# Performance work log

Hardware: AMD Instinct MI355X
Metric: run time of the kernel (lower is better)

## Reference

```python
import jax, jax.numpy as jnp
import numpy as np

B, S, D = 4, 2048, 1024
H = 8
HD = D // H            # 128 head dim
FF = 4096 // H         # 512 per-head expert hidden
E = 8                  # num experts
K = 2                  # top-k
MU, GAMMA = 0.7, 1.0
LN_EPS = 1e-5


def setup_inputs() -> dict:
    key = jax.random.key(0)
    ks = jax.random.split(key, 12)
    sc = lambda *shape: 1.0 / np.sqrt(shape[0])
    return {
        "x": jax.random.normal(ks[0], (B, S, D), jnp.float32),
        "momentum": jnp.zeros((B * S * H, HD), jnp.float32),
        # split proj (input_dim -> input_dim)
        "split_W": jax.random.normal(ks[1], (D, D), jnp.float32) * sc(D),
        "split_b": jnp.zeros((D,), jnp.float32),
        # gate (head_dim -> num_experts)
        "gate_W": jax.random.normal(ks[2], (HD, E), jnp.float32) * sc(HD),
        "gate_b": jnp.zeros((E,), jnp.float32),
        # stacked experts: Linear(HD->FF) ReLU Linear(FF->HD)
        "W1": jax.random.normal(ks[3], (E, HD, FF), jnp.float32) * sc(HD),
        "b1": jnp.zeros((E, FF), jnp.float32),
        "W2": jax.random.normal(ks[4], (E, FF, HD), jnp.float32) * sc(FF),
        "b2": jnp.zeros((E, HD), jnp.float32),
        # layernorm over head_dim
        "ln_g": jnp.ones((HD,), jnp.float32),
        "ln_b": jnp.zeros((HD,), jnp.float32),
        # merge proj
        "merge_W": jax.random.normal(ks[5], (D, D), jnp.float32) * sc(D),
        "merge_b": jnp.zeros((D,), jnp.float32),
    }


def _topk_gate(t, gate_W, gate_b):
    # t: [T, HD] -> dense gate weights [T, E] with only top-K nonzero
    logits = t @ gate_W + gate_b                       # [T, E]
    topv, topi = jax.lax.top_k(logits, K)              # [T, K]
    gates_k = jax.nn.softmax(topv, axis=-1)            # softmax over kept experts
    onehot = jax.nn.one_hot(topi, E, dtype=t.dtype)    # [T, K, E]
    return jnp.einsum("tk,tke->te", gates_k, onehot)   # scatter back


def reference(x, momentum, split_W, split_b, gate_W, gate_b,
              W1, b1, W2, b2, ln_g, ln_b, merge_W, merge_b):
    # split: [B,S,D] -> [B*S*H, HD]
    x_hat = x @ split_W + split_b
    t = x_hat.reshape(B * S * H, HD)

    gates = _topk_gate(t, gate_W, gate_b)              # [T, E]

    # all-experts dense compute (matches the source's per-expert loop)
    h = jax.nn.relu(jnp.einsum("td,edf->etf", t, W1) + b1[:, None, :])  # [E,T,FF]
    eo = jnp.einsum("etf,efd->etd", h, W2) + b2[:, None, :]             # [E,T,HD]
    expert_outputs = jnp.einsum("te,etd->td", gates, eo)                # [T,HD]

    new_momentum = -expert_outputs + MU * momentum
    out = t + GAMMA * new_momentum

    # layernorm over head_dim
    mean = out.mean(-1, keepdims=True)
    var = out.var(-1, keepdims=True)
    out = (out - mean) * jax.lax.rsqrt(var + LN_EPS) * ln_g + ln_b

    # merge: [T,HD] -> [B,S,D] -> linear
    o = out.reshape(B, S, D)
    final = o @ merge_W + merge_b
    return final, new_momentum
```

## Files before the change

### kernel.cpp

```cpp
#include <hip/hip_runtime.h>

#define NBATCH 4
#define NS 2048
#define ND 1024
#define NH 8
#define HD 128
#define NFF 512
#define NE 8
#define NT 65536
#define NBS 8192
#define MU_F 0.7f
#define LN_EPS_F 1e-5f

typedef __attribute__((ext_vector_type(4))) float f32x4;
typedef __attribute__((ext_vector_type(2))) double f64x2;
typedef __attribute__((ext_vector_type(8))) _Float16 f16x8;
typedef __attribute__((ext_vector_type(4))) _Float16 f16x4;
typedef __attribute__((ext_vector_type(2))) _Float16 f16x2;

__device__ __forceinline__ void gload_lds16(const void* g, void* l) {
  __builtin_amdgcn_global_load_lds(
      (const __attribute__((address_space(1))) unsigned int*)g,
      (__attribute__((address_space(3))) unsigned int*)l, 16, 0, 0);
}

__global__ void zero_cnt_kernel(int* cnt) {
  cnt[threadIdx.x] = 0;
}

__global__ void tr_cvt_kernel(const float* __restrict__ in, _Float16* __restrict__ out, int R, int C) {
  __shared__ float tile[32][33];
  int b = blockIdx.z;
  const float* inp = in + (size_t)b * R * C;
  _Float16* outp = out + (size_t)b * R * C;
  int c = blockIdx.x * 32 + threadIdx.x;
  int r0 = blockIdx.y * 32;
  #pragma unroll
  for (int i = 0; i < 4; i++) {
    int r = r0 + threadIdx.y + i * 8;
    tile[threadIdx.y + i * 8][threadIdx.x] = inp[(size_t)r * C + c];
  }
  __syncthreads();
  int rr = r0 + threadIdx.x;
  #pragma unroll
  for (int i = 0; i < 4; i++) {
    int cc = blockIdx.x * 32 + threadIdx.y + i * 8;
    outp[(size_t)cc * R + rr] = (_Float16)tile[threadIdx.x][threadIdx.y + i * 8];
  }
}

__global__ void build_G_kernel(const float* __restrict__ split_W, const float* __restrict__ split_b,
                               const float* __restrict__ gate_W, const float* __restrict__ gate_b,
                               f64x2* __restrict__ Gx2, double* __restrict__ gbias) {
  int idx = blockIdx.x * 256 + threadIdx.x;
  int kp = idx >> 6, o = idx & 63, h = o >> 3, e = o & 7;
  int d0 = kp * 2;
  double a0 = 0.0, a1 = 0.0;
  const float* r0 = split_W + (size_t)d0 * ND + h * 128;
  const float* r1 = r0 + ND;
  for (int j = 0; j < 128; j++) {
    double w = (double)gate_W[j * 8 + e];
    a0 += (double)r0[j] * w;
    a1 += (double)r1[j] * w;
  }
  f64x2 gv = { a0, a1 };
  Gx2[idx] = gv;
  if (idx < 64) {
    double bacc = 0.0;
    for (int j = 0; j < 128; j++)
      bacc += (double)split_b[h * 128 + j] * (double)gate_W[j * 8 + e];
    gbias[idx] = bacc + (double)gate_b[e];
  }
}

__global__ __launch_bounds__(256) void gate_kernel(const float* __restrict__ x,
    const f64x2* __restrict__ Gx2, const double* __restrict__ gbias,
    _Float16* __restrict__ x_h,
    float* __restrict__ tkw, int* __restrict__ lists, int* __restrict__ cnt) {
  __shared__ double xsd[16][66];
  __shared__ double lg[16 * 64];
  __shared__ int lcnt[8];
  __shared__ int lbase[8];
  int tid = threadIdx.x, lane = tid & 63, w = tid >> 6;
  int bs0 = blockIdx.x * 16;
  double acc[4];
  #pragma unroll
  for (int r = 0; r < 4; r++) acc[r] = 0.0;
  int xrow = tid >> 4, xc4 = tid & 15;
  const double* xr = &xsd[0][0] + (w * 4) * 66;
  if (tid < 8) lcnt[tid] = 0;

  for (int ch = 0; ch < 16; ch++) {
    __syncthreads();
    float4 xv4 = *(const float4*)(x + (size_t)(bs0 + xrow) * ND + ch * 64 + xc4 * 4);
    f64x2 xa = { (double)xv4.x, (double)xv4.y };
    f64x2 xb = { (double)xv4.z, (double)xv4.w };
    *(f64x2*)&xsd[xrow][xc4 * 4]     = xa;
    *(f64x2*)&xsd[xrow][xc4 * 4 + 2] = xb;
    f16x4 xh = { (_Float16)xv4.x, (_Float16)xv4.y, (_Float16)xv4.z, (_Float16)xv4.w };
    *(f16x4*)(x_h + (size_t)(bs0 + xrow) * ND + ch * 64 + xc4 * 4) = xh;
    __syncthreads();
    const f64x2* Gc = Gx2 + (size_t)(ch * 32) * 64 + lane;
    #pragma unroll 8
    for (int kp = 0; kp < 32; kp++) {
      f64x2 g = Gc[kp * 64];
      #pragma unroll
      for (int r = 0; r < 4; r++) {
        f64x2 xv = *(const f64x2*)(xr + r * 66 + kp * 2);
        acc[r] += xv.x * g.x;
        acc[r] += xv.y * g.y;
      }
    }
  }
  double gb = gbias[lane];
  #pragma unroll
  for (int r = 0; r < 4; r++)
    lg[(w * 4 + r) * 64 + lane] = acc[r] + gb;
  __syncthreads();

  int i1 = 0, i2 = 0, token = 0, p1 = 0, p2 = 0;
  if (tid < 128) {
    int row = tid >> 3, h = tid & 7;
    const double* L = lg + row * 64 + h * 8;
    double v1 = L[0];
    #pragma unroll
    for (int e2 = 1; e2 < 8; e2++) if (L[e2] > v1) { v1 = L[e2]; i1 = e2; }
    i2 = -1; double v2 = -1e300;
    #pragma unroll
    for (int e2 = 0; e2 < 8; e2++) if (e2 != i1 && L[e2] > v2) { v2 = L[e2]; i2 = e2; }
    float ex = expf((float)(v2 - v1));
    float den = 1.f + ex;
    float g1 = 1.f / den, g2 = ex / den;
    token = (bs0 + row) * 8 + h;
    tkw[token * 2]     = g1;
    tkw[token * 2 + 1] = g2;
    p1 = atomicAdd(&lcnt[i1], 1);
    p2 = atomicAdd(&lcnt[i2], 1);
  }
  __syncthreads();
  if (tid < 8) lbase[tid] = atomicAdd(cnt + tid * 64, lcnt[tid]);
  __syncthreads();
  if (tid < 128) {
    lists[(size_t)i1 * NT + lbase[i1] + p1] = token * 2;
    lists[(size_t)i2 * NT + lbase[i2] + p2] = token * 2 + 1;
  }
}

__global__ __launch_bounds__(256) void gemm_f16_kernel(
    const _Float16* __restrict__ A, const _Float16* __restrict__ Bt,
    const float* __restrict__ bias, float* __restrict__ Cf, _Float16* __restrict__ Ch,
    int M, int N, int Kd) {
  __shared__ _Float16 As[128 * 32];
  __shared__ _Float16 Bs[128 * 32];
  int tid = threadIdx.x, lane = tid & 63, w = tid >> 6;
  int wr = w >> 1, wc = w & 1;
  int m0 = blockIdx.y * 128, n0 = blockIdx.x * 128;
  f32x4 acc[4][4];
  #pragma unroll
  for (int i = 0; i < 4; i++)
    #pragma unroll
    for (int j = 0; j < 4; j++) acc[i][j] = (f32x4){0.f, 0.f, 0.f, 0.f};
  int srow = lane >> 2, scol = (lane & 3) * 8;
  int fr = lane & 15, ko = (lane >> 4) * 8;
  const _Float16* Ag = A + (size_t)(m0 + srow) * Kd + scol;
  const _Float16* Bg = Bt + (size_t)(n0 + srow) * Kd + scol;

  for (int k0 = 0; k0 < Kd; k0 += 32) {
    #pragma unroll
    for (int j = 0; j < 2; j++) {
      int rb = (w * 2 + j) * 16;
      gload_lds16(Ag + (size_t)rb * Kd + k0, As + rb * 32);
      gload_lds16(Bg + (size_t)rb * Kd + k0, Bs + rb * 32);
    }
    __syncthreads();
    f16x8 af[4], bq[4];
    #pragma unroll
    for (int mi = 0; mi < 4; mi++) af[mi] = *(const f16x8*)(As + (wr * 64 + mi * 16 + fr) * 32 + ko);
    #pragma unroll
    for (int ni = 0; ni < 4; ni++) bq[ni] = *(const f16x8*)(Bs + (wc * 64 + ni * 16 + fr) * 32 + ko);
    __syncthreads();
    #pragma unroll
    for (int mi = 0; mi < 4; mi++)
      #pragma unroll
      for (int ni = 0; ni < 4; ni++)
        acc[mi][ni] = __builtin_amdgcn_mfma_f32_16x16x32_f16(af[mi], bq[ni], acc[mi][ni], 0, 0, 0);
  }
  int rbase = m0 + wr * 64 + ((lane >> 4) << 2);
  int cbase = n0 + wc * 64 + (lane & 15);
  #pragma unroll
  for (int mi = 0; mi < 4; mi++)
    #pragma unroll
    for (int ni = 0; ni < 4; ni++) {
      int cc = cbase + ni * 16;
      float bv = bias ? bias[cc] : 0.f;
      #pragma unroll
      for (int r = 0; r < 4; r++) {
        int rr = rbase + mi * 16 + r;
        float v = acc[mi][ni][r] + bv;
        if (Cf) Cf[(size_t)rr * N + cc] = v;
        if (Ch) Ch[(size_t)rr * N + cc] = (_Float16)v;
      }
    }
}

__global__ __launch_bounds__(512, 2) void expert_kernel(
    const _Float16* __restrict__ t_h, const _Float16* __restrict__ W1t, const _Float16* __restrict__ W2t,
    const float* __restrict__ b1, const float* __restrict__ b2,
    const int* __restrict__ cnt, const int* __restrict__ lists, const float* __restrict__ tkw,
    _Float16* __restrict__ slots) {
  int e = blockIdx.x & 7;
  int m0 = (blockIdx.x >> 3) * 128;
  int count = cnt[e * 64];
  if (m0 >= count) return;
  __shared__ _Float16 Wb1[64 * 128];
  __shared__ _Float16 Wb2[128 * 64];
  __shared__ _Float16 h_s[128 * 64];
  __shared__ int alist[128];
  __shared__ float aw[128];
  int tid = threadIdx.x, lane = tid & 63, w = tid >> 6;
  int wr = w >> 1, wc = w & 1;
  int fr = lane & 15, g = lane >> 4;

  if (tid < 128) {
    int idx = m0 + tid;
    int a = (idx < count) ? lists[(size_t)e * NT + idx] : -1;
    alist[tid] = a;
    aw[tid] = (a >= 0) ? tkw[a] : 0.f;
  }
  __syncthreads();

  auto issue_w1 = [&](int ch) {
    #pragma unroll
    for (int j = 0; j < 2; j++) {
      int n = j * 512 + tid;
      int r = n >> 4, gg = n & 15;
      int sg = gg ^ ((r >> 1) & 7);
      const _Float16* src = W1t + (size_t)e * (NFF * HD) + (size_t)(ch * 64 + r) * HD + sg * 8;
      gload_lds16(src, (_Float16*)Wb1 + n * 8);
    }
  };
  auto issue_w2 = [&](int ch) {
    #pragma unroll
    for (int j = 0; j < 2; j++) {
      int n = j * 512 + tid;
      int r = n >> 3, gg = n & 7;
      int sg = gg ^ ((r >> 1) & 7);
      const _Float16* src = W2t + (size_t)e * (HD * NFF) + (size_t)r * NFF + ch * 64 + sg * 8;
      gload_lds16(src, (_Float16*)Wb2 + n * 8);
    }
  };

  issue_w1(0);
  f16x8 af[2][4];
  #pragma unroll
  for (int mi = 0; mi < 2; mi++) {
    int rloc = wr * 32 + mi * 16 + fr;
    int a = alist[rloc];
    const _Float16* tb = t_h + (size_t)(a >> 1) * HD;
    #pragma unroll
    for (int ks = 0; ks < 4; ks++) {
      f16x8 v = {0, 0, 0, 0, 0, 0, 0, 0};
      if (a >= 0) v = *(const f16x8*)(tb + ks * 32 + g * 8);
      af[mi][ks] = v;
    }
  }
  float b2v[4];
  #pragma unroll
  for (int ni = 0; ni < 4; ni++)
    b2v[ni] = b2[e * HD + wc * 64 + ni * 16 + fr];

  __syncthreads();

  f32x4 acc2[2][4];
  #pragma unroll
  for (int i = 0; i < 2; i++)
    #pragma unroll
    for (int j = 0; j < 4; j++) acc2[i][j] = (f32x4){0.f, 0.f, 0.f, 0.f};

  for (int ch = 0; ch < 8; ch++) {
    issue_w2(ch);
    float b1v[2];
    #pragma unroll
    for (int ni = 0; ni < 2; ni++)
      b1v[ni] = b1[e * NFF + ch * 64 + wc * 32 + ni * 16 + fr];
    f32x4 acc1[2][2];
    #pragma unroll
    for (int i = 0; i < 2; i++)
      #pragma unroll
      for (int j = 0; j < 2; j++) acc1[i][j] = (f32x4){0.f, 0.f, 0.f, 0.f};
    #pragma unroll
    for (int ks = 0; ks < 4; ks++) {
      f16x8 bq[2];
      #pragma unroll
      for (int ni = 0; ni < 2; ni++) {
        int rw = wc * 32 + ni * 16 + fr;
        int byte = rw * 256 + ((ks * 64 + g * 16) ^ (((rw >> 1) & 7) << 4));
        bq[ni] = *(const f16x8*)((const char*)Wb1 + byte);
      }
      #pragma unroll
      for (int mi = 0; mi < 2; mi++)
        #pragma unroll
        for (int ni = 0; ni < 2; ni++)
          acc1[mi][ni] = __builtin_amdgcn_mfma_f32_16x16x32_f16(af[mi][ks], bq[ni], acc1[mi][ni], 0, 0, 0);
    }
    #pragma unroll
    for (int mi = 0; mi < 2; mi++)
      #pragma unroll
      for (int ni = 0; ni < 2; ni++) {
        int hc = wc * 32 + ni * 16 + fr;
        #pragma unroll
        for (int r = 0; r < 4; r++) {
          int hr = wr * 32 + mi * 16 + g * 4 + r;
          int byte = hr * 128 + ((hc * 2) ^ (((hr >> 1) & 7) << 4));
          *(_Float16*)((char*)h_s + byte) = (_Float16)fmaxf(acc1[mi][ni][r] + b1v[ni], 0.f);
        }
      }
    __syncthreads();
    if (ch < 7) issue_w1(ch + 1);
    #pragma unroll
    for (int ks = 0; ks < 2; ks++) {
      f16x8 ah[2], bq[4];
      #pragma unroll
      for (int mi = 0; mi < 2; mi++) {
        int row = wr * 32 + mi * 16 + fr;
        int byte = row * 128 + ((ks * 64 + g * 16) ^ (((row >> 1) & 7) << 4));
        ah[mi] = *(const f16x8*)((const char*)h_s + byte);
      }
      #pragma unroll
      for (int ni = 0; ni < 4; ni++) {
        int rw = wc * 64 + ni * 16 + fr;
        int byte = rw * 128 + ((ks * 64 + g * 16) ^ (((rw >> 1) & 7) << 4));
        bq[ni] = *(const f16x8*)((const char*)Wb2 + byte);
      }
      #pragma unroll
      for (int mi = 0; mi < 2; mi++)
        #pragma unroll
        for (int ni = 0; ni < 4; ni++)
          acc2[mi][ni] = __builtin_amdgcn_mfma_f32_16x16x32_f16(ah[mi], bq[ni], acc2[mi][ni], 0, 0, 0);
    }
    __syncthreads();
  }
  #pragma unroll
  for (int mi = 0; mi < 2; mi++)
    #pragma unroll
    for (int ni = 0; ni < 4; ni++) {
      int ncol = wc * 64 + ni * 16 + fr;
      #pragma unroll
      for (int r = 0; r < 4; r++) {
        int m = wr * 32 + mi * 16 + g * 4 + r;
        int a = alist[m];
        if (a >= 0)
          slots[(size_t)a * HD + ncol] = (_Float16)(aw[m] * (acc2[mi][ni][r] + b2v[ni]));
      }
    }
}

__global__ __launch_bounds__(256) void combine_ln_kernel(
    const _Float16* __restrict__ slots, const float* __restrict__ momentum,
    const _Float16* __restrict__ t_h, const float* __restrict__ ln_g, const float* __restrict__ ln_b,
    float* __restrict__ nm_out, _Float16* __restrict__ out_h) {
  int w = threadIdx.x >> 6, lane = threadIdx.x & 63;
  int tok = blockIdx.x * 4 + w;
  int d0 = lane * 2;
  f16x2 s0 = *(const f16x2*)(slots + (size_t)tok * 256 + d0);
  f16x2 s1 = *(const f16x2*)(slots + (size_t)tok * 256 + 128 + d0);
  float2 mo = *(const float2*)(momentum + (size_t)tok * HD + d0);
  f16x2 tv = *(const f16x2*)(t_h + (size_t)tok * HD + d0);
  float nm0 = -((float)s0.x + (float)s1.x) + MU_F * mo.x;
  float nm1 = -((float)s0.y + (float)s1.y) + MU_F * mo.y;
  float2 nm2; nm2.x = nm0; nm2.y = nm1;
  *(float2*)(nm_out + (size_t)tok * HD + d0) = nm2;
  float r0 = (float)tv.x + nm0;
  float r1 = (float)tv.y + nm1;
  float s = r0 + r1, sq = r0 * r0 + r1 * r1;
  #pragma unroll
  for (int m = 1; m < 64; m <<= 1) { s += __shfl_xor(s, m, 64); sq += __shfl_xor(sq, m, 64); }
  float mean = s * (1.f / 128.f);
  float var = sq * (1.f / 128.f) - mean * mean;
  float is = rsqrtf(var + LN_EPS_F);
  float y0 = (r0 - mean) * is * ln_g[d0] + ln_b[d0];
  float y1 = (r1 - mean) * is * ln_g[d0 + 1] + ln_b[d0 + 1];
  f16x2 yo = { (_Float16)y0, (_Float16)y1 };
  *(f16x2*)(out_h + (size_t)tok * HD + d0) = yo;
}

extern "C" void kernel_launch(void* const* d_in, const int* in_sizes, int n_in,
                              void* d_out, int out_size, void* d_ws, size_t ws_size,
                              hipStream_t stream) {
  const float* x        = (const float*)d_in[0];
  const float* momentum = (const float*)d_in[1];
  const float* split_W  = (const float*)d_in[2];
  const float* split_b  = (const float*)d_in[3];
  const float* gate_W   = (const float*)d_in[4];
  const float* gate_b   = (const float*)d_in[5];
  const float* W1       = (const float*)d_in[6];
  const float* b1       = (const float*)d_in[7];
  const float* W2       = (const float*)d_in[8];
  const float* b2       = (const float*)d_in[9];
  const float* ln_g     = (const float*)d_in[10];
  const float* ln_b     = (const float*)d_in[11];
  const float* merge_W  = (const float*)d_in[12];
  const float* merge_b  = (const float*)d_in[13];
  float* final_out = (float*)d_out;
  float* nm_out    = final_out + (size_t)NBS * ND;

  char* ws = (char*)d_ws;
  size_t off = 0;
  auto alloc = [&](size_t bytes) { void* p = ws + off; off = (off + bytes + 255) & ~(size_t)255; return p; };
  _Float16* x_h   = (_Float16*)alloc((size_t)NBS * ND * 2);
  _Float16* t_h   = (_Float16*)alloc((size_t)NT * HD * 2);
  _Float16* out_h = (_Float16*)alloc((size_t)NT * HD * 2);
  _Float16* sWt   = (_Float16*)alloc((size_t)ND * ND * 2);
  _Float16* mWt   = (_Float16*)alloc((size_t)ND * ND * 2);
  _Float16* W1t   = (_Float16*)alloc((size_t)NE * HD * NFF * 2);
  _Float16* W2t   = (_Float16*)alloc((size_t)NE * HD * NFF * 2);
  f64x2*    Gx2   = (f64x2*)alloc((size_t)512 * 64 * 16);
  double*   gbias = (double*)alloc(64 * 8);
  float*    tkw   = (float*)alloc((size_t)NT * 2 * 4);
  int*      lists = (int*)alloc((size_t)NE * NT * 4);
  int*      cnt   = (int*)alloc(512 * 4);
  _Float16* slots = (_Float16*)alloc((size_t)NT * 2 * HD * 2);
  (void)in_sizes; (void)n_in; (void)out_size; (void)ws_size;

  zero_cnt_kernel<<<1, 512, 0, stream>>>(cnt);
  tr_cvt_kernel<<<dim3(32, 32, 1), dim3(32, 8), 0, stream>>>(split_W, sWt, ND, ND);
  tr_cvt_kernel<<<dim3(32, 32, 1), dim3(32, 8), 0, stream>>>(merge_W, mWt, ND, ND);
  tr_cvt_kernel<<<dim3(16, 4, 8), dim3(32, 8), 0, stream>>>(W1, W1t, HD, NFF);
  tr_cvt_kernel<<<dim3(4, 16, 8), dim3(32, 8), 0, stream>>>(W2, W2t, NFF, HD);
  build_G_kernel<<<128, 256, 0, stream>>>(split_W, split_b, gate_W, gate_b, Gx2, gbias);
  gate_kernel<<<512, 256, 0, stream>>>(x, Gx2, gbias, x_h, tkw, lists, cnt);
  gemm_f16_kernel<<<dim3(8, 64), 256, 0, stream>>>(x_h, sWt, split_b, nullptr, t_h, NBS, ND, ND);
  expert_kernel<<<NE * 512, 512, 0, stream>>>(t_h, W1t, W2t, b1, b2, cnt, lists, tkw, slots);
  combine_ln_kernel<<<NT / 4, 256, 0, stream>>>(slots, momentum, t_h, ln_g, ln_b, nm_out, out_h);
  gemm_f16_kernel<<<dim3(8, 64), 256, 0, stream>>>(out_h, mWt, merge_b, final_out, nullptr, NBS, ND, ND);
}
```

Baseline: 250.8 us.

## Pipeline expert weight loads through a three-slot LDS ring with raw waitcnt barriers

Replaces the separate W1/W2 LDS buffers with a three-stage ring that holds alternating W1 and W2 chunks. Each load is issued two phases ahead, and hand-written s_waitcnt vmcnt/barrier sequences take the place of __syncthreads, so global-to-LDS copies overlap with MFMA work. Biases b1 and b2 are staged into shared memory once instead of being read from global memory inside the loop. The cost is more LDS per block, which may lower occupancy, and the manual vmcnt accounting is fragile.

```diff
diff --git a/kernel.cpp b/kernel.cpp
--- a/kernel.cpp
+++ b/kernel.cpp
@@ -212,9 +212,10 @@
   int m0 = (blockIdx.x >> 3) * 128;
   int count = cnt[e * 64];
   if (m0 >= count) return;
-  __shared__ _Float16 Wb1[64 * 128];
-  __shared__ _Float16 Wb2[128 * 64];
+  __shared__ _Float16 ring[3][64 * 128];
   __shared__ _Float16 h_s[128 * 64];
+  __shared__ float b1s[NFF];
+  __shared__ float b2s[HD];
   __shared__ int alist[128];
   __shared__ float aw[128];
   int tid = threadIdx.x, lane = tid & 63, w = tid >> 6;
@@ -227,30 +228,33 @@
     alist[tid] = a;
     aw[tid] = (a >= 0) ? tkw[a] : 0.f;
   }
+  b1s[tid] = b1[e * NFF + tid];
+  if (tid < 128) b2s[tid] = b2[e * HD + tid];
   __syncthreads();
 
-  auto issue_w1 = [&](int ch) {
-    #pragma unroll
-    for (int j = 0; j < 2; j++) {
-      int n = j * 512 + tid;
-      int r = n >> 4, gg = n & 15;
-      int sg = gg ^ ((r >> 1) & 7);
-      const _Float16* src = W1t + (size_t)e * (NFF * HD) + (size_t)(ch * 64 + r) * HD + sg * 8;
-      gload_lds16(src, (_Float16*)Wb1 + n * 8);
+  auto stage = [&](int p) {
+    if (p >= 16) return;
+    int ch = p >> 1;
+    _Float16* dst = &ring[p % 3][0];
+    if ((p & 1) == 0) {
+      #pragma unroll
+      for (int j = 0; j < 2; j++) {
+        int n = j * 512 + tid;
+        int r = n >> 4, gg = n & 15;
+        int sg = gg ^ ((r >> 1) & 7);
+        gload_lds16(W1t + (size_t)e * (NFF * HD) + (size_t)(ch * 64 + r) * HD + sg * 8, dst + n * 8);
+      }
+    } else {
+      #pragma unroll
+      for (int j = 0; j < 2; j++) {
+        int n = j * 512 + tid;
+        int r = n >> 3, gg = n & 7;
+        int sg = gg ^ ((r >> 1) & 7);
+        gload_lds16(W2t + (size_t)e * (HD * NFF) + (size_t)r * NFF + ch * 64 + sg * 8, dst + n * 8);
+      }
     }
   };
-  auto issue_w2 = [&](int ch) {
-    #pragma unroll
-    for (int j = 0; j < 2; j++) {
-      int n = j * 512 + tid;
-      int r = n >> 3, gg = n & 7;
-      int sg = gg ^ ((r >> 1) & 7);
-      const _Float16* src = W2t + (size_t)e * (HD * NFF) + (size_t)r * NFF + ch * 64 + sg * 8;
-      gload_lds16(src, (_Float16*)Wb2 + n * 8);
-    }
-  };
-
-  issue_w1(0);
+
   f16x8 af[2][4];
   #pragma unroll
   for (int mi = 0; mi < 2; mi++) {
@@ -264,12 +268,9 @@
       af[mi][ks] = v;
     }
   }
-  float b2v[4];
-  #pragma unroll
-  for (int ni = 0; ni < 4; ni++)
-    b2v[ni] = b2[e * HD + wc * 64 + ni * 16 + fr];
-
-  __syncthreads();
+  asm volatile("s_waitcnt vmcnt(0)" ::: "memory");
+  stage(0); stage(1);
+  asm volatile("s_waitcnt vmcnt(2) lgkmcnt(0)\n\ts_barrier" ::: "memory");
 
   f32x4 acc2[2][4];
   #pragma unroll
@@ -277,80 +278,89 @@
     #pragma unroll
     for (int j = 0; j < 4; j++) acc2[i][j] = (f32x4){0.f, 0.f, 0.f, 0.f};
 
-  for (int ch = 0; ch < 8; ch++) {
-    issue_w2(ch);
-    float b1v[2];
-    #pragma unroll
-    for (int ni = 0; ni < 2; ni++)
-      b1v[ni] = b1[e * NFF + ch * 64 + wc * 32 + ni * 16 + fr];
-    f32x4 acc1[2][2];
-    #pragma unroll
-    for (int i = 0; i < 2; i++)
-      #pragma unroll
-      for (int j = 0; j < 2; j++) acc1[i][j] = (f32x4){0.f, 0.f, 0.f, 0.f};
-    #pragma unroll
-    for (int ks = 0; ks < 4; ks++) {
-      f16x8 bq[2];
-      #pragma unroll
-      for (int ni = 0; ni < 2; ni++) {
-        int rw = wc * 32 + ni * 16 + fr;
-        int byte = rw * 256 + ((ks * 64 + g * 16) ^ (((rw >> 1) & 7) << 4));
-        bq[ni] = *(const f16x8*)((const char*)Wb1 + byte);
+  #pragma unroll
+  for (int p = 0; p < 16; p++) {
+    stage(p + 2);
+    int ch = p >> 1;
+    const char* WB = (const char*)&ring[p % 3][0];
+    if ((p & 1) == 0) {
+      float b1v[2];
+      #pragma unroll
+      for (int ni = 0; ni < 2; ni++)
+        b1v[ni] = b1s[ch * 64 + wc * 32 + ni * 16 + fr];
+      f32x4 acc1[2][2];
+      #pragma unroll
+      for (int i = 0; i < 2; i++)
+        #pragma unroll
+        for (int j = 0; j < 2; j++) acc1[i][j] = (f32x4){0.f, 0.f, 0.f, 0.f};
+      #pragma unroll
+      for (int ks = 0; ks < 4; ks++) {
+        f16x8 bq[2];
+        #pragma unroll
+        for (int ni = 0; ni < 2; ni++) {
+          int rw = wc * 32 + ni * 16 + fr;
+          int byte = rw * 256 + ((ks * 64 + g * 16) ^ (((rw >> 1) & 7) << 4));
+          bq[ni] = *(const f16x8*)(WB + byte);
+        }
+        #pragma unroll
+        for (int mi = 0; mi < 2; mi++)
+          #pragma unroll
+          for (int ni = 0; ni < 2; ni++)
+            acc1[mi][ni] = __builtin_amdgcn_mfma_f32_16x16x32_f16(af[mi][ks], bq[ni], acc1[mi][ni], 0, 0, 0);
       }
       #pragma unroll
       for (int mi = 0; mi < 2; mi++)
         #pragma unroll
-        for (int ni = 0; ni < 2; ni++)
-          acc1[mi][ni] = __builtin_amdgcn_mfma_f32_16x16x32_f16(af[mi][ks], bq[ni], acc1[mi][ni], 0, 0, 0);
-    }
-    #pragma unroll
-    for (int mi = 0; mi < 2; mi++)
-      #pragma unroll
-      for (int ni = 0; ni < 2; ni++) {
-        int hc = wc * 32 + ni * 16 + fr;
-        #pragma unroll
-        for (int r = 0; r < 4; r++) {
-          int hr = wr * 32 + mi * 16 + g * 4 + r;
-          int byte = hr * 128 + ((hc * 2) ^ (((hr >> 1) & 7) << 4));
-          *(_Float16*)((char*)h_s + byte) = (_Float16)fmaxf(acc1[mi][ni][r] + b1v[ni], 0.f);
+        for (int ni = 0; ni < 2; ni++) {
+          int hc = wc * 32 + ni * 16 + fr;
+          #pragma unroll
+          for (int r = 0; r < 4; r++) {
+            int hr = wr * 32 + mi * 16 + g * 4 + r;
+            int byte = hr * 128 + ((hc * 2) ^ (((hr >> 1) & 7) << 4));
+            *(_Float16*)((char*)h_s + byte) = (_Float16)fmaxf(acc1[mi][ni][r] + b1v[ni], 0.f);
+          }
         }
-      }
-    __syncthreads();
-    if (ch < 7) issue_w1(ch + 1);
-    #pragma unroll
-    for (int ks = 0; ks < 2; ks++) {
-      f16x8 ah[2], bq[4];
-      #pragma unroll
-      for (int mi = 0; mi < 2; mi++) {
-        int row = wr * 32 + mi * 16 + fr;
-        int byte = row * 128 + ((ks * 64 + g * 16) ^ (((row >> 1) & 7) << 4));
-        ah[mi] = *(const f16x8*)((const char*)h_s + byte);
-      }
-      #pragma unroll
-      for (int ni = 0; ni < 4; ni++) {
-        int rw = wc * 64 + ni * 16 + fr;
-        int byte = rw * 128 + ((ks * 64 + g * 16) ^ (((rw >> 1) & 7) << 4));
-        bq[ni] = *(const f16x8*)((const char*)Wb2 + byte);
-      }
-      #pragma unroll
-      for (int mi = 0; mi < 2; mi++)
-        #pragma unroll
-        for (int ni = 0; ni < 4; ni++)
-          acc2[mi][ni] = __builtin_amdgcn_mfma_f32_16x16x32_f16(ah[mi], bq[ni], acc2[mi][ni], 0, 0, 0);
-    }
-    __syncthreads();
+    } else {
+      #pragma unroll
+      for (int ks = 0; ks < 2; ks++) {
+        f16x8 ah[2], bq[4];
+        #pragma unroll
+        for (int mi = 0; mi < 2; mi++) {
+          int row = wr * 32 + mi * 16 + fr;
+          int byte = row * 128 + ((ks * 64 + g * 16) ^ (((row >> 1) & 7) << 4));
+          ah[mi] = *(const f16x8*)((const char*)h_s + byte);
+        }
+        #pragma unroll
+        for (int ni = 0; ni < 4; ni++) {
+          int rw = wc * 64 + ni * 16 + fr;
+          int byte = rw * 128 + ((ks * 64 + g * 16) ^ (((rw >> 1) & 7) << 4));
+          bq[ni] = *(const f16x8*)((const char*)&ring[p % 3][0] + byte);
+        }
+        #pragma unroll
+        for (int mi = 0; mi < 2; mi++)
+          #pragma unroll
+          for (int ni = 0; ni < 4; ni++)
+            acc2[mi][ni] = __builtin_amdgcn_mfma_f32_16x16x32_f16(ah[mi], bq[ni], acc2[mi][ni], 0, 0, 0);
+      }
+    }
+    if (p == 14) {
+      asm volatile("s_waitcnt vmcnt(0) lgkmcnt(0)\n\ts_barrier" ::: "memory");
+    } else if (p < 14) {
+      asm volatile("s_waitcnt vmcnt(2) lgkmcnt(0)\n\ts_barrier" ::: "memory");
+    }
   }
   #pragma unroll
   for (int mi = 0; mi < 2; mi++)
     #pragma unroll
     for (int ni = 0; ni < 4; ni++) {
       int ncol = wc * 64 + ni * 16 + fr;
+      float bv = b2s[ncol];
       #pragma unroll
       for (int r = 0; r < 4; r++) {
         int m = wr * 32 + mi * 16 + g * 4 + r;
         int a = alist[m];
         if (a >= 0)
-          slots[(size_t)a * HD + ncol] = (_Float16)(aw[m] * (acc2[mi][ni][r] + b2v[ni]));
+          slots[(size_t)a * HD + ncol] = (_Float16)(aw[m] * (acc2[mi][ni][r] + bv));
       }
     }
 }
```

New measurement: 247.8 us. Within noise of the previous version (-1.2%).
